# Kernel tuning notes

Measured on AMD Instinct MI355X. Metric: run time of the kernel, lower is better.

The kernel has to match this reference:

```python
import jax, jax.numpy as jnp
import numpy as np

B, S, D, H = 2, 2048, 1024, 16
HD = D // H  # 64


def setup_inputs() -> dict:
    key = jax.random.key(0)
    ks = jax.random.split(key, 5)
    sc = 1.0 / np.sqrt(D)
    return {
        "x": jax.random.normal(ks[0], (B, S, D), jnp.float32),
        "wq": jax.random.normal(ks[1], (D, D), jnp.float32) * sc,
        "bq": jnp.zeros((D,), jnp.float32),
        "wk": jax.random.normal(ks[2], (D, D), jnp.float32) * sc,
        "bk": jnp.zeros((D,), jnp.float32),
        "wv": jax.random.normal(ks[3], (D, D), jnp.float32) * sc,
        "bv": jnp.zeros((D,), jnp.float32),
        "wo": jax.random.normal(ks[4], (D, D), jnp.float32) * sc,
        "bo": jnp.zeros((D,), jnp.float32),
    }


def _rope_tables(seq_len, dim):
    inv_freq = 1.0 / (10000.0 ** (jnp.arange(0, dim, 2, dtype=jnp.float32) / dim))
    t = jnp.arange(seq_len, dtype=jnp.float32)
    freqs = jnp.einsum("i,j->ij", t, inv_freq)  # [S, dim/2]
    emb = jnp.concatenate([freqs, freqs], axis=-1)  # [S, dim]
    return jnp.cos(emb)[None, None], jnp.sin(emb)[None, None]  # [1,1,S,dim]


def _rotate_half(x):
    x1, x2 = x[..., : x.shape[-1] // 2], x[..., x.shape[-1] // 2 :]
    return jnp.concatenate([-x2, x1], axis=-1)


def reference(x, wq, bq, wk, bk, wv, bv, wo, bo):
    b, s, d = x.shape
    h, hd = H, d // H
    # projections (torch Linear: x @ W.T + b) -> [b, h, s, hd]
    def proj(w, bias):
        return (x @ w.T + bias).reshape(b, s, h, hd).transpose(0, 2, 1, 3)

    q, k, v = proj(wq, bq), proj(wk, bk), proj(wv, bv)
    cos, sin = _rope_tables(s, hd)
    q = q * cos + _rotate_half(q) * sin
    k = k * cos + _rotate_half(k) * sin
    scores = jnp.einsum("bhqd,bhkd->bhqk", q, k) / jnp.sqrt(jnp.float32(hd))
    attn = jax.nn.softmax(scores, axis=-1)
    out = jnp.einsum("bhqk,bhkd->bhqd", attn, v)
    out = out.transpose(0, 2, 1, 3).reshape(b, s, d)
    return out @ wo.T + bo
```

## Files before the change

kernel.cpp:

```cpp
#include <hip/hip_runtime.h>
#include <hip/hip_bf16.h>

#define Bq 2
#define Sq 2048
#define Dq 1024
#define Hq 16
#define QSCALE 0.18033688011112042f

typedef __attribute__((ext_vector_type(8))) short short8;
typedef __attribute__((ext_vector_type(4))) float floatx4;
typedef unsigned short ushort_t;

#define VMCNT0() asm volatile("s_waitcnt vmcnt(0)" ::: "memory")
#define GLDS(src, dst) __builtin_amdgcn_global_load_lds( \
    (const __attribute__((address_space(1))) void*)(src), \
    (__attribute__((address_space(3))) void*)(dst), 16, 0, 0)

__device__ __forceinline__ ushort_t f2bf(float f) {
    union { float f; unsigned u; } v; v.f = f;
    unsigned u = v.u;
    u += 0x7fffu + ((u >> 16) & 1u);
    return (ushort_t)(u >> 16);
}

__device__ __forceinline__ unsigned pk_bf16(float a, float b) {
    union { __hip_bfloat162 h; unsigned u; } c;
    c.h = __float22bfloat162_rn(float2{a, b});
    return c.u;
}

__device__ __forceinline__ void cvt8(const float* __restrict__ in, ushort_t* __restrict__ out, int i) {
    const float4* p = (const float4*)in + (size_t)i * 2;
    float4 a = p[0], b = p[1];
    ushort4 lo, hi;
    lo.x = f2bf(a.x); lo.y = f2bf(a.y); lo.z = f2bf(a.z); lo.w = f2bf(a.w);
    hi.x = f2bf(b.x); hi.y = f2bf(b.y); hi.z = f2bf(b.z); hi.w = f2bf(b.w);
    *(ushort4*)(out + (size_t)i * 8)     = lo;
    *(ushort4*)(out + (size_t)i * 8 + 4) = hi;
}

__global__ void prep(const float* __restrict__ x,
                     const float* __restrict__ wq, const float* __restrict__ wk,
                     const float* __restrict__ wv, const float* __restrict__ wo,
                     ushort_t* __restrict__ xb,
                     ushort_t* __restrict__ wqb, ushort_t* __restrict__ wkb,
                     ushort_t* __restrict__ wvb, ushort_t* __restrict__ wob,
                     float* __restrict__ cost, float* __restrict__ sint) {
    int b = blockIdx.x;
    if (b < 2048) {
        cvt8(x, xb, b * 256 + threadIdx.x);
    } else if (b < 4096) {
        int w = (b - 2048) >> 9;
        int i = ((b - 2048) & 511) * 256 + threadIdx.x;
        const float* src = (w == 0) ? wq : (w == 1) ? wk : (w == 2) ? wv : wo;
        ushort_t* dst    = (w == 0) ? wqb : (w == 1) ? wkb : (w == 2) ? wvb : wob;
        cvt8(src, dst, i);
    } else {
        int i = (b - 4096) * 256 + threadIdx.x;
        int s = i >> 5, f = i & 31;
        float invf = powf(10000.0f, -(float)f / 32.0f);
        float ang = (float)s * invf;
        cost[i] = cosf(ang);
        sint[i] = sinf(ang);
    }
}

__global__ __launch_bounds__(256, 3) void gemm_qkv(
    const ushort_t* __restrict__ xb,
    const ushort_t* __restrict__ wqb, const ushort_t* __restrict__ wkb, const ushort_t* __restrict__ wvb,
    const float* __restrict__ bq, const float* __restrict__ bk, const float* __restrict__ bv,
    const float* __restrict__ cost, const float* __restrict__ sint,
    ushort_t* __restrict__ qout, ushort_t* __restrict__ kout, ushort_t* __restrict__ vtout)
{
    __shared__ ushort_t As0[128 * 32], As1[128 * 32];
    __shared__ ushort_t Bs0[128 * 32], Bs1[128 * 32];
    const int mode = blockIdx.z;
    const ushort_t* W  = (mode == 0) ? wqb : (mode == 1) ? wkb : wvb;
    const float* bias  = (mode == 0) ? bq  : (mode == 1) ? bk  : bv;

    const int t = threadIdx.x;
    const int lane = t & 63;
    const int wid = t >> 6;
    const int l15 = lane & 15, lk = lane >> 4;
    const int wr = wid >> 1, wc = wid & 1;
    const int rowBase = blockIdx.y * 128;
    const int colBase = blockIdx.x * 128;

    floatx4 acc[4][4] = {};

    const char* aSrc[2];
    const char* bSrc[2];
    int ldso[2];
#pragma unroll
    for (int issue = 0; issue < 2; ++issue) {
        int ldsoff = issue * 4096 + t * 16;
        int row = ldsoff >> 6;
        int cb  = ldsoff & 63;
        ldso[issue] = ldsoff;
        aSrc[issue] = (const char*)xb + (size_t)(rowBase + row) * 2048 + cb;
        bSrc[issue] = (const char*)W  + (size_t)(colBase + row) * 2048 + cb;
    }

    auto STAGE = [&](ushort_t* Ad, ushort_t* Bd) {
#pragma unroll
        for (int issue = 0; issue < 2; ++issue) {
            GLDS(aSrc[issue], (char*)Ad + ldso[issue]);
            GLDS(bSrc[issue], (char*)Bd + ldso[issue]);
        }
        aSrc[0] += 64; aSrc[1] += 64; bSrc[0] += 64; bSrc[1] += 64;
    };

    auto KSTEP = [&](const ushort_t* Ac, const ushort_t* Bc, int knext, ushort_t* An, ushort_t* Bn) {
        if (knext < Dq) STAGE(An, Bn);
        short8 a[4], b[4];
#pragma unroll
        for (int m = 0; m < 4; ++m)
            a[m] = *(const short8*)((const char*)Ac + (wr * 64 + m * 16 + l15) * 64 + lk * 16);
#pragma unroll
        for (int n = 0; n < 4; ++n)
            b[n] = *(const short8*)((const char*)Bc + (wc * 64 + n * 16 + l15) * 64 + lk * 16);
        __builtin_amdgcn_s_setprio(1);
#pragma unroll
        for (int m = 0; m < 4; ++m)
#pragma unroll
            for (int n = 0; n < 4; ++n)
                acc[m][n] = __builtin_amdgcn_mfma_f32_16x16x32_bf16(a[m], b[n], acc[m][n], 0, 0, 0);
        __builtin_amdgcn_s_setprio(0);
        VMCNT0();
        __syncthreads();
    };

    STAGE(As0, Bs0);
    VMCNT0();
    __syncthreads();

#pragma unroll 1
    for (int k0 = 0; k0 < Dq; k0 += 64) {
        KSTEP(As0, Bs0, k0 + 32, As1, Bs1);
        KSTEP(As1, Bs1, k0 + 64, As0, Bs0);
    }

    const int colW = colBase + wc * 64;
    const int hh = colW >> 6;

    if (mode < 2) {
        ushort_t* outp = (mode == 0) ? qout : kout;
        const float osc = (mode == 0) ? QSCALE : 1.0f;
#pragma unroll
        for (int m = 0; m < 4; ++m) {
            int rg0 = rowBase + wr * 64 + m * 16 + lk * 4;
#pragma unroll
            for (int n2 = 0; n2 < 2; ++n2) {
                int d0 = n2 * 16 + l15;
                float b0 = bias[colW + d0];
                float b2 = bias[colW + d0 + 32];
#pragma unroll
                for (int r = 0; r < 4; ++r) {
                    int rg = rg0 + r;
                    int bb = rg >> 11;
                    int s  = rg & 2047;
                    float c  = cost[s * 32 + d0];
                    float sn = sint[s * 32 + d0];
                    float a0 = acc[m][n2][r]     + b0;
                    float a2 = acc[m][n2 + 2][r] + b2;
                    float o0 = (a0 * c - a2 * sn) * osc;
                    float o2 = (a2 * c + a0 * sn) * osc;
                    size_t base = ((size_t)(bb * Hq + hh) * Sq + s) * 64;
                    outp[base + d0]      = f2bf(o0);
                    outp[base + d0 + 32] = f2bf(o2);
                }
            }
        }
    } else {
#pragma unroll
        for (int m = 0; m < 4; ++m) {
            int rg0 = rowBase + wr * 64 + m * 16 + lk * 4;
            int bb  = rg0 >> 11;
            int s0  = rg0 & 2047;
            int g   = (s0 & 63) >> 2;
            int ng  = (g >> 3) * 8 + (g & 3) * 2 + ((g >> 2) & 1);
            int s2b = (s0 & ~63) + ng * 4;
#pragma unroll
            for (int n = 0; n < 4; ++n) {
                int d = n * 16 + l15;
                float bb_ = bias[colW + d];
#pragma unroll
                for (int r = 0; r < 4; ++r)
                    vtout[((size_t)(bb * Hq + hh) * 64 + d) * Sq + s2b + r] = f2bf(acc[m][n][r] + bb_);
            }
        }
    }
}

__global__ __launch_bounds__(256, 4) void flash_attn(
    const ushort_t* __restrict__ qbuf, const ushort_t* __restrict__ kbuf,
    const ushort_t* __restrict__ vtbuf, ushort_t* __restrict__ abuf)
{
    __shared__ char Ks0[64 * 128], Ks1[64 * 128];
    __shared__ char Vs0[64 * 128], Vs1[64 * 128];

    const int t = threadIdx.x, lane = t & 63, wid = t >> 6;
    const int l15 = lane & 15, lk = lane >> 4;

    int flat = blockIdx.y * 32 + blockIdx.x;
    flat = (flat & 7) * 128 + (flat >> 3);
    const int qtile = flat & 31, bh = flat >> 5;
    const int bpos = bh >> 4, h = bh & 15;
    const int qbase = qtile * 64 + wid * 16;

    const ushort_t* Qp = qbuf + ((size_t)bh * Sq + qbase) * 64;
    short8 qf[2];
#pragma unroll
    for (int kk = 0; kk < 2; ++kk)
        qf[kk] = *(const short8*)(Qp + l15 * 64 + kk * 32 + lk * 8);

    short8 onesf;
#pragma unroll
    for (int j = 0; j < 8; ++j) onesf[j] = (short)0x3F80;

    floatx4 oacc[4] = {};
    floatx4 lacc = {};

    int off_[4][2];
#pragma unroll
    for (int n = 0; n < 4; ++n) {
        int swz = (l15 & 7) << 4;
#pragma unroll
        for (int kk = 0; kk < 2; ++kk)
            off_[n][kk] = (n * 16 + l15) * 128 + ((kk * 64 + lk * 16) ^ swz);
    }

    const char* Kg = (const char*)kbuf  + (size_t)bh * Sq * 128;
    const char* Vg = (const char*)vtbuf + (size_t)bh * 64 * Sq * 2;
    unsigned kOff[2], vOff[2];
    int ldso[2];
#pragma unroll
    for (int issue = 0; issue < 2; ++issue) {
        int ldsoff = issue * 4096 + t * 16;
        int row = ldsoff >> 7;
        int pb  = ldsoff & 127;
        int lb  = pb ^ ((row & 7) << 4);
        ldso[issue] = ldsoff;
        kOff[issue] = (unsigned)(row * 128 + lb);
        vOff[issue] = (unsigned)(row * 4096 + lb);
    }

    auto STAGE = [&](char* Kd, char* Vd) {
#pragma unroll
        for (int issue = 0; issue < 2; ++issue) {
            GLDS(Kg + kOff[issue], Kd + ldso[issue]);
            GLDS(Vg + vOff[issue], Vd + ldso[issue]);
        }
        kOff[0] += 8192; kOff[1] += 8192; vOff[0] += 128; vOff[1] += 128;
    };

    auto TILE = [&](const char* Kc, const char* Vc, bool doStage, char* Kn, char* Vn) {
        if (doStage) STAGE(Kn, Vn);

        short8 kf[4][2];
#pragma unroll
        for (int n = 0; n < 4; ++n)
#pragma unroll
            for (int kk = 0; kk < 2; ++kk)
                kf[n][kk] = *(const short8*)(Kc + off_[n][kk]);

        floatx4 sacc[4] = {};
        __builtin_amdgcn_s_setprio(1);
#pragma unroll
        for (int kk = 0; kk < 2; ++kk)
#pragma unroll
            for (int n = 0; n < 4; ++n)
                sacc[n] = __builtin_amdgcn_mfma_f32_16x16x32_bf16(kf[n][kk], qf[kk], sacc[n], 0, 0, 0);
        __builtin_amdgcn_s_setprio(0);

        short8 vf[4][2];
#pragma unroll
        for (int n = 0; n < 4; ++n)
#pragma unroll
            for (int kb = 0; kb < 2; ++kb)
                vf[n][kb] = *(const short8*)(Vc + off_[n][kb]);

        float p[4][4];
#pragma unroll
        for (int n = 0; n < 4; ++n)
#pragma unroll
            for (int r = 0; r < 4; ++r)
                p[n][r] = __builtin_exp2f(sacc[n][r]);

        short8 paf[2];
#pragma unroll
        for (int kb = 0; kb < 2; ++kb) {
            union { unsigned u[4]; short8 v; } pu;
            pu.u[0] = pk_bf16(p[2 * kb][0],     p[2 * kb][1]);
            pu.u[1] = pk_bf16(p[2 * kb][2],     p[2 * kb][3]);
            pu.u[2] = pk_bf16(p[2 * kb + 1][0], p[2 * kb + 1][1]);
            pu.u[3] = pk_bf16(p[2 * kb + 1][2], p[2 * kb + 1][3]);
            paf[kb] = pu.v;
        }

        __builtin_amdgcn_s_setprio(1);
#pragma unroll
        for (int kb = 0; kb < 2; ++kb) {
#pragma unroll
            for (int n = 0; n < 4; ++n)
                oacc[n] = __builtin_amdgcn_mfma_f32_16x16x32_bf16(paf[kb], vf[n][kb], oacc[n], 0, 0, 0);
            lacc = __builtin_amdgcn_mfma_f32_16x16x32_bf16(paf[kb], onesf, lacc, 0, 0, 0);
        }
        __builtin_amdgcn_s_setprio(0);

        VMCNT0();
        __syncthreads();
    };

    STAGE(Ks0, Vs0);
    VMCNT0();
    __syncthreads();

#pragma unroll 1
    for (int i = 0; i < 15; ++i) {
        TILE(Ks0, Vs0, true, Ks1, Vs1);
        TILE(Ks1, Vs1, true, Ks0, Vs0);
    }
    TILE(Ks0, Vs0, true,  Ks1, Vs1);
    TILE(Ks1, Vs1, false, Ks0, Vs0);

#pragma unroll
    for (int r = 0; r < 4; ++r) {
        float linv = 1.0f / lacc[r];
        int srow = qbase + lk * 4 + r;
        size_t base = ((size_t)bpos * Sq + srow) * Dq + h * 64;
#pragma unroll
        for (int n = 0; n < 4; ++n)
            abuf[base + n * 16 + l15] = f2bf(oacc[n][r] * linv);
    }
}

__global__ __launch_bounds__(256, 4) void gemm_out(
    const ushort_t* __restrict__ ab, const ushort_t* __restrict__ wob,
    const float* __restrict__ bo, float* __restrict__ out)
{
    __shared__ ushort_t As0[128 * 32], As1[128 * 32];
    __shared__ ushort_t Bs0[64 * 32],  Bs1[64 * 32];
    const int t = threadIdx.x;
    const int lane = t & 63;
    const int wid = t >> 6;
    const int l15 = lane & 15, lk = lane >> 4;
    const int wr = wid >> 1, wc = wid & 1;
    const int rowBase = blockIdx.y * 128;
    const int colBase = blockIdx.x * 64;

    floatx4 acc[4][2] = {};

    const char* aSrc[2];
    const char* bSrc;
    int ldso[2];
#pragma unroll
    for (int issue = 0; issue < 2; ++issue) {
        int ldsoff = issue * 4096 + t * 16;
        int row = ldsoff >> 6;
        int cb  = ldsoff & 63;
        ldso[issue] = ldsoff;
        aSrc[issue] = (const char*)ab + (size_t)(rowBase + row) * 2048 + cb;
    }
    {
        int ldsoff = t * 16;
        int row = ldsoff >> 6;
        int cb  = ldsoff & 63;
        bSrc = (const char*)wob + (size_t)(colBase + row) * 2048 + cb;
    }

    auto STAGE = [&](ushort_t* Ad, ushort_t* Bd) {
#pragma unroll
        for (int issue = 0; issue < 2; ++issue)
            GLDS(aSrc[issue], (char*)Ad + ldso[issue]);
        GLDS(bSrc, (char*)Bd + ldso[0]);
        aSrc[0] += 64; aSrc[1] += 64; bSrc += 64;
    };

    auto KSTEP = [&](const ushort_t* Ac, const ushort_t* Bc, int knext, ushort_t* An, ushort_t* Bn) {
        if (knext < Dq) STAGE(An, Bn);
        short8 a[4], b[2];
#pragma unroll
        for (int m = 0; m < 4; ++m)
            a[m] = *(const short8*)((const char*)Ac + (wr * 64 + m * 16 + l15) * 64 + lk * 16);
#pragma unroll
        for (int n = 0; n < 2; ++n)
            b[n] = *(const short8*)((const char*)Bc + (wc * 32 + n * 16 + l15) * 64 + lk * 16);
        __builtin_amdgcn_s_setprio(1);
#pragma unroll
        for (int m = 0; m < 4; ++m)
#pragma unroll
            for (int n = 0; n < 2; ++n)
                acc[m][n] = __builtin_amdgcn_mfma_f32_16x16x32_bf16(a[m], b[n], acc[m][n], 0, 0, 0);
        __builtin_amdgcn_s_setprio(0);
        VMCNT0();
        __syncthreads();
    };

    STAGE(As0, Bs0);
    VMCNT0();
    __syncthreads();

#pragma unroll 1
    for (int k0 = 0; k0 < Dq; k0 += 64) {
        KSTEP(As0, Bs0, k0 + 32, As1, Bs1);
        KSTEP(As1, Bs1, k0 + 64, As0, Bs0);
    }

    const int colW = colBase + wc * 32;
#pragma unroll
    for (int m = 0; m < 4; ++m) {
        int rg0 = rowBase + wr * 64 + m * 16 + lk * 4;
#pragma unroll
        for (int n = 0; n < 2; ++n) {
            int colg = colW + n * 16 + l15;
            float bb_ = bo[colg];
#pragma unroll
            for (int r = 0; r < 4; ++r)
                out[(size_t)(rg0 + r) * Dq + colg] = acc[m][n][r] + bb_;
        }
    }
}

extern "C" void kernel_launch(void* const* d_in, const int* in_sizes, int n_in,
                              void* d_out, int out_size, void* d_ws, size_t ws_size,
                              hipStream_t stream) {
    (void)in_sizes; (void)n_in; (void)out_size;
    const float* x  = (const float*)d_in[0];
    const float* wq = (const float*)d_in[1];
    const float* bq = (const float*)d_in[2];
    const float* wk = (const float*)d_in[3];
    const float* bk = (const float*)d_in[4];
    const float* wv = (const float*)d_in[5];
    const float* bv = (const float*)d_in[6];
    const float* wo = (const float*)d_in[7];
    const float* bo = (const float*)d_in[8];
    float* out = (float*)d_out;

    if (ws_size < 50855936) return;
    char* ws = (char*)d_ws;
    ushort_t* xb   = (ushort_t*)(ws + 0);
    ushort_t* wqb  = (ushort_t*)(ws + 8388608);
    ushort_t* wkb  = (ushort_t*)(ws + 10485760);
    ushort_t* wvb  = (ushort_t*)(ws + 12582912);
    ushort_t* wob  = (ushort_t*)(ws + 14680064);
    ushort_t* qb   = (ushort_t*)(ws + 16777216);
    ushort_t* kb   = (ushort_t*)(ws + 25165824);
    ushort_t* vtb  = (ushort_t*)(ws + 33554432);
    ushort_t* abuf = (ushort_t*)(ws + 41943040);
    float*    cost = (float*)(ws + 50331648);
    float*    sint = (float*)(ws + 50593792);

    prep<<<4352, 256, 0, stream>>>(x, wq, wk, wv, wo, xb, wqb, wkb, wvb, wob, cost, sint);
    gemm_qkv<<<dim3(8, 32, 3), 256, 0, stream>>>(xb, wqb, wkb, wvb, bq, bk, bv, cost, sint, qb, kb, vtb);
    flash_attn<<<dim3(32, 32), 256, 0, stream>>>(qb, kb, vtb, abuf);
    gemm_out<<<dim3(16, 32), 256, 0, stream>>>(abuf, wob, bo, out);
}
```

Before: 120.9 us.

## Process two query subtiles per wave in flash attention for K/V reuse

Doubles the query tile per block to 128 rows, with each wave computing two 16-row MFMA subtiles against the same K/V fragments loaded from LDS. This halves the K/V global-to-LDS staging and the LDS fragment reads per query row, and halves the grid size. In exchange it raises register pressure (launch bounds lowered to 3 blocks) and reduces the number of blocks available to fill the GPU.

```diff
diff --git a/kernel.cpp b/kernel.cpp
--- a/kernel.cpp
+++ b/kernel.cpp
@@ -192,7 +192,7 @@
     }
 }
 
-__global__ __launch_bounds__(256, 4) void flash_attn(
+__global__ __launch_bounds__(256, 3) void flash_attn(
     const ushort_t* __restrict__ qbuf, const ushort_t* __restrict__ kbuf,
     const ushort_t* __restrict__ vtbuf, ushort_t* __restrict__ abuf)
 {
@@ -202,24 +202,26 @@
     const int t = threadIdx.x, lane = t & 63, wid = t >> 6;
     const int l15 = lane & 15, lk = lane >> 4;
 
-    int flat = blockIdx.y * 32 + blockIdx.x;
-    flat = (flat & 7) * 128 + (flat >> 3);
-    const int qtile = flat & 31, bh = flat >> 5;
+    int flat = blockIdx.y * 16 + blockIdx.x;
+    flat = (flat & 7) * 64 + (flat >> 3);
+    const int qtile = flat & 15, bh = flat >> 4;
     const int bpos = bh >> 4, h = bh & 15;
-    const int qbase = qtile * 64 + wid * 16;
+    const int qbase = qtile * 128 + wid * 32;
 
     const ushort_t* Qp = qbuf + ((size_t)bh * Sq + qbase) * 64;
-    short8 qf[2];
-#pragma unroll
-    for (int kk = 0; kk < 2; ++kk)
-        qf[kk] = *(const short8*)(Qp + l15 * 64 + kk * 32 + lk * 8);
+    short8 qf[2][2];
+#pragma unroll
+    for (int mq = 0; mq < 2; ++mq)
+#pragma unroll
+        for (int kk = 0; kk < 2; ++kk)
+            qf[mq][kk] = *(const short8*)(Qp + (mq * 16 + l15) * 64 + kk * 32 + lk * 8);
 
     short8 onesf;
 #pragma unroll
     for (int j = 0; j < 8; ++j) onesf[j] = (short)0x3F80;
 
-    floatx4 oacc[4] = {};
-    floatx4 lacc = {};
+    floatx4 oacc[2][4] = {};
+    floatx4 lacc[2] = {};
 
     int off_[4][2];
 #pragma unroll
@@ -264,13 +266,15 @@
             for (int kk = 0; kk < 2; ++kk)
                 kf[n][kk] = *(const short8*)(Kc + off_[n][kk]);
 
-        floatx4 sacc[4] = {};
+        floatx4 sacc[2][4] = {};
         __builtin_amdgcn_s_setprio(1);
 #pragma unroll
         for (int kk = 0; kk < 2; ++kk)
 #pragma unroll
             for (int n = 0; n < 4; ++n)
-                sacc[n] = __builtin_amdgcn_mfma_f32_16x16x32_bf16(kf[n][kk], qf[kk], sacc[n], 0, 0, 0);
+#pragma unroll
+                for (int mq = 0; mq < 2; ++mq)
+                    sacc[mq][n] = __builtin_amdgcn_mfma_f32_16x16x32_bf16(kf[n][kk], qf[mq][kk], sacc[mq][n], 0, 0, 0);
         __builtin_amdgcn_s_setprio(0);
 
         short8 vf[4][2];
@@ -280,31 +284,37 @@
             for (int kb = 0; kb < 2; ++kb)
                 vf[n][kb] = *(const short8*)(Vc + off_[n][kb]);
 
-        float p[4][4];
-#pragma unroll
-        for (int n = 0; n < 4; ++n)
-#pragma unroll
-            for (int r = 0; r < 4; ++r)
-                p[n][r] = __builtin_exp2f(sacc[n][r]);
-
-        short8 paf[2];
+        short8 paf[2][2];
+#pragma unroll
+        for (int mq = 0; mq < 2; ++mq) {
+            float p[4][4];
+#pragma unroll
+            for (int n = 0; n < 4; ++n)
+#pragma unroll
+                for (int r = 0; r < 4; ++r)
+                    p[n][r] = __builtin_exp2f(sacc[mq][n][r]);
+#pragma unroll
+            for (int kb = 0; kb < 2; ++kb) {
+                union { unsigned u[4]; short8 v; } pu;
+                pu.u[0] = pk_bf16(p[2 * kb][0],     p[2 * kb][1]);
+                pu.u[1] = pk_bf16(p[2 * kb][2],     p[2 * kb][3]);
+                pu.u[2] = pk_bf16(p[2 * kb + 1][0], p[2 * kb + 1][1]);
+                pu.u[3] = pk_bf16(p[2 * kb + 1][2], p[2 * kb + 1][3]);
+                paf[mq][kb] = pu.v;
+            }
+        }
+
+        __builtin_amdgcn_s_setprio(1);
 #pragma unroll
         for (int kb = 0; kb < 2; ++kb) {
-            union { unsigned u[4]; short8 v; } pu;
-            pu.u[0] = pk_bf16(p[2 * kb][0],     p[2 * kb][1]);
-            pu.u[1] = pk_bf16(p[2 * kb][2],     p[2 * kb][3]);
-            pu.u[2] = pk_bf16(p[2 * kb + 1][0], p[2 * kb + 1][1]);
-            pu.u[3] = pk_bf16(p[2 * kb + 1][2], p[2 * kb + 1][3]);
-            paf[kb] = pu.v;
-        }
-
-        __builtin_amdgcn_s_setprio(1);
-#pragma unroll
-        for (int kb = 0; kb < 2; ++kb) {
 #pragma unroll
             for (int n = 0; n < 4; ++n)
-                oacc[n] = __builtin_amdgcn_mfma_f32_16x16x32_bf16(paf[kb], vf[n][kb], oacc[n], 0, 0, 0);
-            lacc = __builtin_amdgcn_mfma_f32_16x16x32_bf16(paf[kb], onesf, lacc, 0, 0, 0);
+#pragma unroll
+                for (int mq = 0; mq < 2; ++mq)
+                    oacc[mq][n] = __builtin_amdgcn_mfma_f32_16x16x32_bf16(paf[mq][kb], vf[n][kb], oacc[mq][n], 0, 0, 0);
+#pragma unroll
+            for (int mq = 0; mq < 2; ++mq)
+                lacc[mq] = __builtin_amdgcn_mfma_f32_16x16x32_bf16(paf[mq][kb], onesf, lacc[mq], 0, 0, 0);
         }
         __builtin_amdgcn_s_setprio(0);
 
@@ -325,14 +335,16 @@
     TILE(Ks1, Vs1, false, Ks0, Vs0);
 
 #pragma unroll
-    for (int r = 0; r < 4; ++r) {
-        float linv = 1.0f / lacc[r];
-        int srow = qbase + lk * 4 + r;
-        size_t base = ((size_t)bpos * Sq + srow) * Dq + h * 64;
-#pragma unroll
-        for (int n = 0; n < 4; ++n)
-            abuf[base + n * 16 + l15] = f2bf(oacc[n][r] * linv);
-    }
+    for (int mq = 0; mq < 2; ++mq)
+#pragma unroll
+        for (int r = 0; r < 4; ++r) {
+            float linv = 1.0f / lacc[mq][r];
+            int srow = qbase + mq * 16 + lk * 4 + r;
+            size_t base = ((size_t)bpos * Sq + srow) * Dq + h * 64;
+#pragma unroll
+            for (int n = 0; n < 4; ++n)
+                abuf[base + n * 16 + l15] = f2bf(oacc[mq][n][r] * linv);
+        }
 }
 
 __global__ __launch_bounds__(256, 4) void gemm_out(
@@ -453,6 +465,6 @@
 
     prep<<<4352, 256, 0, stream>>>(x, wq, wk, wv, wo, xb, wqb, wkb, wvb, wob, cost, sint);
     gemm_qkv<<<dim3(8, 32, 3), 256, 0, stream>>>(xb, wqb, wkb, wvb, bq, bk, bv, cost, sint, qb, kb, vtb);
-    flash_attn<<<dim3(32, 32), 256, 0, stream>>>(qb, kb, vtb, abuf);
+    flash_attn<<<dim3(16, 32), 256, 0, stream>>>(qb, kb, vtb, abuf);
     gemm_out<<<dim3(16, 32), 256, 0, stream>>>(abuf, wob, bo, out);
 }
```

Measured after the change: 118.9 us. No clear change (-1.6%).
